# Optimization experiments

Measured on AMD Instinct MI355X. Metric: run time of the kernel, lower is better.

## Reference

```python
import jax, jax.numpy as jnp
import numpy as np

SENTENCE_NUMBER = 32
UNITS = 50
WORD_DIM = 100   # 2 * MIDDLE_OUTPUT
USER_DIM = 100   # 2 * USER_VEC_DIM
B, T = 256, 2048


def setup_inputs() -> dict:
    key = jax.random.key(0)
    ks = jax.random.split(key, 6)
    return {
        "sentence_batch": jax.random.normal(ks[0], (B, T, WORD_DIM), dtype=jnp.float32),
        "user_vec_batch": jax.random.normal(ks[1], (B, USER_DIM), dtype=jnp.float32),
        "vw": jax.random.normal(ks[2], (UNITS, 1), dtype=jnp.float32) * 0.05,
        "wh": jax.random.normal(ks[3], (UNITS, WORD_DIM), dtype=jnp.float32) * 0.05,
        "wu": jax.random.normal(ks[4], (UNITS, USER_DIM), dtype=jnp.float32) * 0.05,
        "bw": jax.random.normal(ks[5], (UNITS, 1), dtype=jnp.float32) * 0.05,
    }


def reference(sentence_batch, user_vec_batch, vw, wh, wu, bw):
    # Additive attention per word, softmax within each sentence section,
    # weighted-sum pooling of words -> one vector per sentence.
    b, t, d = sentence_batch.shape
    s = SENTENCE_NUMBER
    sec = t // s
    # batched projections (replaces per-word (units x 1) matmuls)
    wh_proj = jnp.einsum("btd,ud->btu", sentence_batch, wh)          # [B,T,units]
    wu_proj = jnp.einsum("bd,ud->bu", user_vec_batch, wu) + bw[:, 0]  # [B,units]
    tan = jnp.tanh(wh_proj + wu_proj[:, None, :])                    # [B,T,units]
    e = tan @ vw[:, 0]                                               # [B,T]
    # softmax over words within each sentence section
    e = e.reshape(b, s, sec)
    alpha = jax.nn.softmax(e, axis=-1)                               # [B,S,sec]
    words = sentence_batch.reshape(b, s, sec, d)
    # weighted-sum pooling -> document of sentence vectors
    return jnp.einsum("bsw,bswd->bsd", alpha, words)                 # [B,S,D]
```

## Files before the change

### kernel.cpp

```cpp
#include <hip/hip_runtime.h>
#include <hip/hip_bf16.h>

#define B_   256
#define T_   2048
#define D_   100
#define U_   50
#define S_   32
#define SEC_ 64

typedef __attribute__((ext_vector_type(8))) short short8;
typedef __attribute__((ext_vector_type(4))) float f32x4;

__device__ __forceinline__ float fast_tanh(float x) {
    float e = __expf(2.0f * x);
    return 1.0f - 2.0f * __builtin_amdgcn_rcpf(1.0f + e);
}

__device__ __forceinline__ short f2bf(float f) {
    union { __hip_bfloat16 h; unsigned short u; } cv;
    cv.h = __float2bfloat16(f);
    return (short)cv.u;
}

__device__ __forceinline__ short8 pack8(f32x4 a, f32x4 b) {
    short8 r;
    r[0] = f2bf(a[0]); r[1] = f2bf(a[1]); r[2] = f2bf(a[2]); r[3] = f2bf(a[3]);
    r[4] = f2bf(b[0]); r[5] = f2bf(b[1]); r[6] = f2bf(b[2]); r[7] = f2bf(b[3]);
    return r;
}

template<int CTRL>
__device__ __forceinline__ float ror_add(float v) {
    union { float f; int i; } in, out;
    in.f = v;
    out.i = __builtin_amdgcn_update_dpp(0, in.i, CTRL, 0xF, 0xF, true);
    return v + out.f;
}
__device__ __forceinline__ float fold16(float v) {
    v = ror_add<0x128>(v);
    v = ror_add<0x124>(v);
    v = ror_add<0x122>(v);
    v = ror_add<0x121>(v);
    return v;
}

#define LOADY(Y, Y6, mm) do {                                            \
    const float* p_ = secm + 1600 * (mm);                                \
    Y[0] = *reinterpret_cast<const f32x4*>(p_ + 4 * l);                  \
    Y[1] = *reinterpret_cast<const f32x4*>(p_ + 256 + 4 * l);            \
    Y[2] = *reinterpret_cast<const f32x4*>(p_ + 512 + 4 * l);            \
    Y[3] = *reinterpret_cast<const f32x4*>(p_ + 768 + 4 * l);            \
    Y[4] = *reinterpret_cast<const f32x4*>(p_ + 1024 + 4 * l);           \
    Y[5] = *reinterpret_cast<const f32x4*>(p_ + 1280 + 4 * l);           \
    Y6   = p_[1536 + l];                                                 \
} while (0)

#define STAGE_READ(Y, Y6, X) do {                                        \
    _Pragma("unroll")                                                    \
    for (int j = 0; j < 6; ++j)                                          \
        *reinterpret_cast<f32x4*>(sb + 256 * j + 4 * l) = Y[j];          \
    sb[1536 + l] = Y6;                                                   \
    asm volatile("s_waitcnt lgkmcnt(0)" ::: "memory");                   \
    _Pragma("unroll")                                                    \
    for (int j = 0; j < 6; ++j)                                          \
        X[j] = *reinterpret_cast<const f32x4*>(sb + li * 100 + 4 * g + 16 * j); \
    X[6] = *reinterpret_cast<const f32x4*>(sb + li * 100 + 96) * mg;     \
} while (0)

#define COMPUTE_M(X) do {                                                \
    short8 af[4];                                                        \
    af[0] = pack8(X[0], X[1]);                                           \
    af[1] = pack8(X[2], X[3]);                                           \
    af[2] = pack8(X[4], X[5]);                                           \
    af[3] = pack8(X[6], zero4);                                          \
    f32x4 acc[4];                                                        \
    _Pragma("unroll")                                                    \
    for (int n = 0; n < 4; ++n) acc[n] = (f32x4){0.f, 0.f, 0.f, 0.f};    \
    _Pragma("unroll")                                                    \
    for (int ks = 0; ks < 4; ++ks) {                                     \
        _Pragma("unroll")                                                \
        for (int n = 0; n < 4; ++n) {                                    \
            acc[n] = __builtin_amdgcn_mfma_f32_16x16x32_bf16(            \
                whb[n * 4 + ks][l], af[ks], acc[n], 0, 0, 0);            \
        }                                                                \
    }                                                                    \
    f32x4 t[4];                                                          \
    _Pragma("unroll")                                                    \
    for (int n = 0; n < 4; ++n) {                                        \
        _Pragma("unroll")                                                \
        for (int r = 0; r < 4; ++r)                                      \
            t[n][r] = vwl2[n][r] * fast_tanh(acc[n][r] + gl2[n][r]);     \
    }                                                                    \
    f32x4 e4 = (f32x4){0.f, 0.f, 0.f, 0.f};                              \
    e4 = __builtin_amdgcn_mfma_f32_16x16x32_bf16(                        \
        a2ones, pack8(t[0], t[1]), e4, 0, 0, 0);                         \
    e4 = __builtin_amdgcn_mfma_f32_16x16x32_bf16(                        \
        a2ones, pack8(t[2], t[3]), e4, 0, 0, 0);                         \
    const float p = __expf(e4[0] - Mb);                                  \
    tsum += p;                                                           \
    _Pragma("unroll")                                                    \
    for (int j = 0; j < 7; ++j)                                          \
        pool[j] = pool[j] + X[j] * p;                                    \
} while (0)

__global__ __launch_bounds__(256, 2) void attn_pool_v10(
    const float* __restrict__ sent,
    const float* __restrict__ user_vec,
    const float* __restrict__ vw,
    const float* __restrict__ wh,
    const float* __restrict__ wu,
    const float* __restrict__ bw,
    float* __restrict__ out) {
    __shared__ short8 whb[16][64];
    __shared__ __align__(16) float xstage[4][1600];
    __shared__ float wup_s[64];
    __shared__ float poolbuf[4][128];

    const int tid = threadIdx.x;
    const int wid = tid >> 6;
    const int l   = tid & 63;
    const int g   = l >> 4;
    const int li  = l & 15;

    const int b = blockIdx.x >> 3;
    const int s = (blockIdx.x & 7) * 4 + wid;
    const float* secm = sent + ((size_t)b * T_ + (size_t)s * SEC_) * D_;
    float* sb = &xstage[wid][0];

    const float mg = (g == 0) ? 1.f : 0.f;
    const f32x4 zero4 = (f32x4){0.f, 0.f, 0.f, 0.f};

    f32x4 yA[6], yB[6];
    float y6A, y6B;
    LOADY(yA, y6A, 0);
    LOADY(yB, y6B, 1);

#pragma unroll
    for (int j = 0; j < 4; ++j) {
        const int idx = tid + 256 * j;
        const int pli = idx & 15;
        const int pg  = (idx >> 4) & 3;
        const int pks = (idx >> 6) & 3;
        const int pn  = idx >> 8;
        const int u   = 16 * pn + pli;
        const bool uv = (u < U_);
        const int k0  = 32 * pks + 4 * pg;
        const bool v1 = uv && (k0 <= D_ - 4);
        const bool v2 = uv && (k0 + 16 <= D_ - 4);
        const float* rowp = wh + (uv ? u : 0) * D_;
        f32x4 a  = *reinterpret_cast<const f32x4*>(rowp + (v1 ? k0 : 0));
        f32x4 bb = *reinterpret_cast<const f32x4*>(rowp + (v2 ? k0 + 16 : 0));
        a  *= (v1 ? 1.f : 0.f);
        bb *= (v2 ? 1.f : 0.f);
        whb[idx >> 6][idx & 63] = pack8(a, bb);
    }

    if (tid < U_) {
        const f32x4* uv4 = reinterpret_cast<const f32x4*>(user_vec + b * D_);
        const f32x4* wu4 = reinterpret_cast<const f32x4*>(wu + tid * D_);
        float acc = 0.f;
#pragma unroll
        for (int c = 0; c < D_ / 4; ++c) {
            f32x4 a = uv4[c];
            f32x4 w = wu4[c];
            acc = __builtin_fmaf(a[0], w[0], acc);
            acc = __builtin_fmaf(a[1], w[1], acc);
            acc = __builtin_fmaf(a[2], w[2], acc);
            acc = __builtin_fmaf(a[3], w[3], acc);
        }
        wup_s[tid] = acc + bw[tid];
    }

    f32x4 vwl2[4];
#pragma unroll
    for (int n = 0; n < 4; ++n) {
#pragma unroll
        for (int r = 0; r < 4; ++r) {
            const int uu = 16 * n + 4 * g + r;
            const bool uv = (uu < U_);
            vwl2[n][r] = uv ? vw[uu] : 0.f;
        }
    }
    float Mb = 0.f;
#pragma unroll
    for (int n = 0; n < 4; ++n)
#pragma unroll
        for (int r = 0; r < 4; ++r) Mb += fabsf(vwl2[n][r]);
    Mb += __shfl_xor(Mb, 16);
    Mb += __shfl_xor(Mb, 32);

    short8 a2ones;
#pragma unroll
    for (int i = 0; i < 8; ++i) a2ones[i] = (short)0x3F80;

    __syncthreads();

    f32x4 gl2[4];
#pragma unroll
    for (int n = 0; n < 4; ++n) {
#pragma unroll
        for (int r = 0; r < 4; ++r) {
            const int uu = 16 * n + 4 * g + r;
            gl2[n][r] = (uu < U_) ? wup_s[uu] : 0.f;
        }
    }

    f32x4 pool[7];
#pragma unroll
    for (int j = 0; j < 7; ++j) pool[j] = zero4;
    float tsum = 0.f;

    f32x4 X[7];
    STAGE_READ(yA, y6A, X);
    LOADY(yA, y6A, 2);
    COMPUTE_M(X);

    STAGE_READ(yB, y6B, X);
    LOADY(yB, y6B, 3);
    COMPUTE_M(X);

    STAGE_READ(yA, y6A, X);
    COMPUTE_M(X);

    STAGE_READ(yB, y6B, X);
    COMPUTE_M(X);

    const float inv = 1.0f / fold16(tsum);
#pragma unroll
    for (int j = 0; j < 7; ++j) {
#pragma unroll
        for (int c = 0; c < 4; ++c) pool[j][c] = fold16(pool[j][c]);
    }

    if (li == 0) {
#pragma unroll
        for (int j = 0; j < 6; ++j) {
#pragma unroll
            for (int c = 0; c < 4; ++c) {
                const int k = 32 * (j >> 1) + 16 * (j & 1) + 4 * g + c;
                poolbuf[wid][k] = pool[j][c];
            }
        }
        if (g == 0) {
#pragma unroll
            for (int c = 0; c < 4; ++c) poolbuf[wid][96 + c] = pool[6][c];
        }
    }
    asm volatile("s_waitcnt lgkmcnt(0)" ::: "memory");

    float* po = out + ((size_t)b * S_ + s) * D_;
    po[l] = poolbuf[wid][l] * inv;
    if (l < D_ - SEC_) po[SEC_ + l] = poolbuf[wid][SEC_ + l] * inv;
}

extern "C" void kernel_launch(void* const* d_in, const int* in_sizes, int n_in,
                              void* d_out, int out_size, void* d_ws, size_t ws_size,
                              hipStream_t stream) {
    const float* sent = (const float*)d_in[0];
    const float* uvec = (const float*)d_in[1];
    const float* vw   = (const float*)d_in[2];
    const float* wh   = (const float*)d_in[3];
    const float* wu   = (const float*)d_in[4];
    const float* bw   = (const float*)d_in[5];
    float* out = (float*)d_out;

    attn_pool_v10<<<dim3(B_ * S_ / 4), dim3(256), 0, stream>>>(
        sent, uvec, vw, wh, wu, bw, out);
}
```

Baseline: 42.70 us.

## Process two sentence sections per wave to amortize per-block setup

Each wave now handles two consecutive sentence sections instead of one, which halves the grid. The double-buffered global loads run continuously across both sections, and an epilogue writes out each section in turn. The goal is to amortize the per-block setup (the wh bf16 conversion, the wu projection and the syncthreads) and keep load prefetching going across section boundaries. The cost is fewer blocks in flight, so latency hiding and occupancy on the GPU could suffer.

```diff
diff --git a/kernel.cpp b/kernel.cpp
--- a/kernel.cpp
+++ b/kernel.cpp
@@ -44,8 +44,8 @@
     return v;
 }
 
-#define LOADY(Y, Y6, mm) do {                                            \
-    const float* p_ = secm + 1600 * (mm);                                \
+#define LOADY(Y, Y6, qq) do {                                            \
+    const float* p_ = secm + 1600 * (qq);                                \
     Y[0] = *reinterpret_cast<const f32x4*>(p_ + 4 * l);                  \
     Y[1] = *reinterpret_cast<const f32x4*>(p_ + 256 + 4 * l);            \
     Y[2] = *reinterpret_cast<const f32x4*>(p_ + 512 + 4 * l);            \
@@ -103,7 +103,39 @@
         pool[j] = pool[j] + X[j] * p;                                    \
 } while (0)
 
-__global__ __launch_bounds__(256, 2) void attn_pool_v10(
+#define EPILOG(PO) do {                                                  \
+    const float inv_ = 1.0f / fold16(tsum);                              \
+    _Pragma("unroll")                                                    \
+    for (int j = 0; j < 7; ++j) {                                        \
+        _Pragma("unroll")                                                \
+        for (int c = 0; c < 4; ++c) pool[j][c] = fold16(pool[j][c]);     \
+    }                                                                    \
+    if (li == 0) {                                                       \
+        _Pragma("unroll")                                                \
+        for (int j = 0; j < 6; ++j) {                                    \
+            _Pragma("unroll")                                            \
+            for (int c = 0; c < 4; ++c) {                                \
+                const int k = 32 * (j >> 1) + 16 * (j & 1) + 4 * g + c;  \
+                poolbuf[wid][k] = pool[j][c];                            \
+            }                                                            \
+        }                                                                \
+        if (g == 0) {                                                    \
+            _Pragma("unroll")                                            \
+            for (int c = 0; c < 4; ++c) poolbuf[wid][96 + c] = pool[6][c]; \
+        }                                                                \
+    }                                                                    \
+    asm volatile("s_waitcnt lgkmcnt(0)" ::: "memory");                   \
+    {                                                                    \
+        float* po_ = (PO);                                               \
+        po_[l] = poolbuf[wid][l] * inv_;                                 \
+        if (l < D_ - SEC_) po_[SEC_ + l] = poolbuf[wid][SEC_ + l] * inv_; \
+    }                                                                    \
+    _Pragma("unroll")                                                    \
+    for (int j = 0; j < 7; ++j) pool[j] = zero4;                         \
+    tsum = 0.f;                                                          \
+} while (0)
+
+__global__ __launch_bounds__(256, 2) void attn_pool_v11(
     const float* __restrict__ sent,
     const float* __restrict__ user_vec,
     const float* __restrict__ vw,
@@ -122,9 +154,10 @@
     const int g   = l >> 4;
     const int li  = l & 15;
 
-    const int b = blockIdx.x >> 3;
-    const int s = (blockIdx.x & 7) * 4 + wid;
-    const float* secm = sent + ((size_t)b * T_ + (size_t)s * SEC_) * D_;
+    const int W  = blockIdx.x * 4 + wid;
+    const int b  = W >> 4;
+    const int sp = W & 15;
+    const float* secm = sent + ((size_t)b * T_ + (size_t)(2 * sp) * SEC_) * D_;
     float* sb = &xstage[wid][0];
 
     const float mg = (g == 0) ? 1.f : 0.f;
@@ -177,8 +210,7 @@
 #pragma unroll
         for (int r = 0; r < 4; ++r) {
             const int uu = 16 * n + 4 * g + r;
-            const bool uv = (uu < U_);
-            vwl2[n][r] = uv ? vw[uu] : 0.f;
+            vwl2[n][r] = (uu < U_) ? vw[uu] : 0.f;
         }
     }
     float Mb = 0.f;
@@ -210,47 +242,24 @@
     for (int j = 0; j < 7; ++j) pool[j] = zero4;
     float tsum = 0.f;
 
+    float* po = out + ((size_t)b * S_ + 2 * sp) * D_;
     f32x4 X[7];
-    STAGE_READ(yA, y6A, X);
-    LOADY(yA, y6A, 2);
-    COMPUTE_M(X);
-
-    STAGE_READ(yB, y6B, X);
-    LOADY(yB, y6B, 3);
-    COMPUTE_M(X);
-
-    STAGE_READ(yA, y6A, X);
-    COMPUTE_M(X);
-
-    STAGE_READ(yB, y6B, X);
-    COMPUTE_M(X);
-
-    const float inv = 1.0f / fold16(tsum);
-#pragma unroll
-    for (int j = 0; j < 7; ++j) {
-#pragma unroll
-        for (int c = 0; c < 4; ++c) pool[j][c] = fold16(pool[j][c]);
-    }
-
-    if (li == 0) {
-#pragma unroll
-        for (int j = 0; j < 6; ++j) {
-#pragma unroll
-            for (int c = 0; c < 4; ++c) {
-                const int k = 32 * (j >> 1) + 16 * (j & 1) + 4 * g + c;
-                poolbuf[wid][k] = pool[j][c];
-            }
-        }
-        if (g == 0) {
-#pragma unroll
-            for (int c = 0; c < 4; ++c) poolbuf[wid][96 + c] = pool[6][c];
-        }
-    }
-    asm volatile("s_waitcnt lgkmcnt(0)" ::: "memory");
-
-    float* po = out + ((size_t)b * S_ + s) * D_;
-    po[l] = poolbuf[wid][l] * inv;
-    if (l < D_ - SEC_) po[SEC_ + l] = poolbuf[wid][SEC_ + l] * inv;
+
+#pragma unroll
+    for (int q = 0; q < 8; q += 2) {
+        STAGE_READ(yA, y6A, X);
+        if (q + 2 < 8) LOADY(yA, y6A, q + 2);
+        COMPUTE_M(X);
+
+        STAGE_READ(yB, y6B, X);
+        if (q + 3 < 8) LOADY(yB, y6B, q + 3);
+        COMPUTE_M(X);
+
+        if ((q & 3) == 2) {
+            EPILOG(po);
+            po += D_;
+        }
+    }
 }
 
 extern "C" void kernel_launch(void* const* d_in, const int* in_sizes, int n_in,
@@ -264,6 +273,6 @@
     const float* bw   = (const float*)d_in[5];
     float* out = (float*)d_out;
 
-    attn_pool_v10<<<dim3(B_ * S_ / 4), dim3(256), 0, stream>>>(
+    attn_pool_v11<<<dim3(B_ * S_ / 8), dim3(256), 0, stream>>>(
         sent, uvec, vw, wh, wu, bw, out);
 }
```

Result: no change. 41.97 us (-1.7%).
